# Kernel tuning notes

Measured on AMD Instinct MI355X. Metric: run time of the kernel, lower is better.

## Reference

```python
import jax, jax.numpy as jnp
import numpy as np

N, E, D, H, C, L = 100000, 1280000, 64, 4, 16, 3  # nodes, edges, dim, heads, head_dim, layers
NEG_SLOPE = 0.2
LN_EPS = 1e-5


def setup_inputs() -> dict:
    key = jax.random.key(0)
    ks = jax.random.split(key, 6)
    scale = 1.0 / np.sqrt(D)
    x = jax.random.normal(ks[0], (N, D), dtype=jnp.float32)
    edge_index = jax.random.randint(ks[1], (2, E), 0, N, dtype=jnp.int64)
    Wl = jax.random.normal(ks[2], (L, D, H * C), dtype=jnp.float32) * scale  # lin_l (source)
    Wr = jax.random.normal(ks[3], (L, D, H * C), dtype=jnp.float32) * scale  # lin_r (target)
    att = jax.random.normal(ks[4], (L, H, C), dtype=jnp.float32) * scale
    bias = jnp.zeros((L, H * C), dtype=jnp.float32)
    gamma = jnp.ones((L, D), dtype=jnp.float32)
    beta = jnp.zeros((L, D), dtype=jnp.float32)
    return dict(x=x, edge_index=edge_index, Wl=Wl, Wr=Wr, att=att, bias=bias, gamma=gamma, beta=beta)


def _gatv2_conv(x, src, dst, Wl, Wr, att, bias):
    # GATv2Conv (concat=True, share_weights=False, negative_slope=0.2)
    n = x.shape[0]
    xl = (x @ Wl).reshape(n, H, C)  # messages from source nodes
    xr = (x @ Wr).reshape(n, H, C)  # target-side transform
    m = xl[src] + xr[dst]  # [E', H, C]
    e = jnp.einsum('ehc,hc->eh', jax.nn.leaky_relu(m, NEG_SLOPE), att)  # [E', H]
    emax = jax.ops.segment_max(e, dst, num_segments=n)
    p = jnp.exp(e - emax[dst])
    denom = jax.ops.segment_sum(p, dst, num_segments=n)
    alpha = p / denom[dst]  # self-loops guarantee denom > 0
    out = jax.ops.segment_sum(alpha[:, :, None] * xl[src], dst, num_segments=n)  # [N, H, C]
    return out.reshape(n, H * C) + bias


def _layernorm(x, gamma, beta):
    mu = jnp.mean(x, axis=-1, keepdims=True)
    var = jnp.mean(jnp.square(x - mu), axis=-1, keepdims=True)
    return (x - mu) * jax.lax.rsqrt(var + LN_EPS) * gamma + beta


def reference(x, edge_index, Wl, Wr, att, bias, gamma, beta):
    n = x.shape[0]
    loops = jnp.arange(n, dtype=edge_index.dtype)
    src = jnp.concatenate([edge_index[0], loops])  # PyG add_self_loops=True
    dst = jnp.concatenate([edge_index[1], loops])
    for i in range(L):
        x_res = x
        x = _gatv2_conv(x, src, dst, Wl[i], Wr[i], att[i], bias[i])
        x = x + x_res  # residual
        x = _layernorm(x, gamma[i], beta[i])
        x = jax.nn.gelu(x, approximate=False)
    return x
```

## Files before the change

kernel.cpp:

```cpp
#include <hip/hip_runtime.h>
#include <math.h>


#define SCAN_CHUNK 1024

typedef __attribute__((ext_vector_type(8))) short short8;
typedef __attribute__((ext_vector_type(4))) float f32x4;

static inline int cdiv(int a, int b) { return (a + b - 1) / b; }

__device__ __forceinline__ unsigned short bf16_rtn(float v) {
    unsigned u = __float_as_uint(v);
    return (unsigned short)((u + 0x7fffu + ((u >> 16) & 1u)) >> 16);
}


__global__ void csr_init(const unsigned int* __restrict__ ei, int* __restrict__ flag,
                         int* __restrict__ deg, int N) {
    int i = blockIdx.x * blockDim.x + threadIdx.x;
    if (i < N) deg[i] = 1;
    if (blockIdx.x == 0 && threadIdx.x < 64) {
        int nz = (ei[2 * threadIdx.x + 1] != 0u) ? 1 : 0;
        unsigned long long b = __ballot(nz);
        if (threadIdx.x == 0) *flag = (b == 0ull) ? 1 : 0;
    }
}

__global__ void hist_kernel(const int* __restrict__ ei, int E, const int* __restrict__ flag,
                            int* __restrict__ deg, int* __restrict__ pos) {
    int e = blockIdx.x * blockDim.x + threadIdx.x;
    if (e >= E) return;
    int is64 = *flag;
    int d = is64 ? ei[2 * (E + e)] : ei[E + e];
    pos[e] = atomicAdd(&deg[d], 1);
}

__global__ void scan_blocks(const int* __restrict__ deg, int* __restrict__ rowptr,
                            int* __restrict__ partials, int N) {
    __shared__ int sdata[256];
    int t = threadIdx.x;
    int idx0 = blockIdx.x * SCAN_CHUNK + t * 4;
    int v[4]; int sum = 0;
    #pragma unroll
    for (int i = 0; i < 4; ++i) {
        int ii = idx0 + i;
        v[i] = (ii < N) ? deg[ii] : 0;
        sum += v[i];
    }
    sdata[t] = sum;
    __syncthreads();
    for (int off = 1; off < 256; off <<= 1) {
        int val = 0;
        if (t >= off) val = sdata[t - off];
        __syncthreads();
        if (t >= off) sdata[t] += val;
        __syncthreads();
    }
    int run = (t > 0) ? sdata[t - 1] : 0;
    #pragma unroll
    for (int i = 0; i < 4; ++i) {
        int ii = idx0 + i;
        if (ii < N) rowptr[ii] = run;
        run += v[i];
    }
    if (t == 255) partials[blockIdx.x] = sdata[255];
}

__global__ void scan_partials_k(int* __restrict__ partials, int NB) {
    __shared__ int sd[256];
    int t = threadIdx.x;
    sd[t] = (t < NB) ? partials[t] : 0;
    __syncthreads();
    for (int off = 1; off < 256; off <<= 1) {
        int val = 0;
        if (t >= off) val = sd[t - off];
        __syncthreads();
        if (t >= off) sd[t] += val;
        __syncthreads();
    }
    if (t < NB) partials[t] = (t > 0) ? sd[t - 1] : 0;
}

__global__ void add_offsets(int* __restrict__ rowptr, const int* __restrict__ partials,
                            int N, int Etot) {
    int i = blockIdx.x * blockDim.x + threadIdx.x;
    if (i < N) rowptr[i] += partials[i / SCAN_CHUNK];
    if (i == 0) rowptr[N] = Etot;
}

__global__ void fill_csr(const int* __restrict__ ei, int E, int N, const int* __restrict__ flag,
                         const int* __restrict__ rowptr, const int* __restrict__ pos,
                         int* __restrict__ col) {
    int i = blockIdx.x * blockDim.x + threadIdx.x;
    if (i >= E + N) return;
    if (i < E) {
        int is64 = *flag;
        int s = is64 ? ei[2 * i] : ei[i];
        int d = is64 ? ei[2 * (E + i)] : ei[E + i];
        col[rowptr[d] + pos[i]] = s;
    } else {
        int nn = i - E;
        col[rowptr[nn]] = nn;
    }
}

__global__ void wprep_kernel(const float* __restrict__ Wl, const float* __restrict__ Wr,
                             unsigned short* __restrict__ Bh, int Lnum) {
    int t = blockIdx.x * blockDim.x + threadIdx.x;
    int total = Lnum * 2 * 4 * 2 * 64 * 8;
    if (t >= total) return;
    int j    = t & 7;
    int lane = (t >> 3) & 63;
    int kc   = (t >> 9) & 1;
    int ct   = (t >> 10) & 3;
    int h    = (t >> 12) & 1;
    int l    = t >> 13;
    const float* W = (h ? Wr : Wl) + (size_t)l * 4096;
    int k = kc * 32 + (lane >> 4) * 8 + j;
    int c = ct * 16 + (lane & 15);
    Bh[t] = bf16_rtn(W[k * 64 + c]);
}

__global__ __launch_bounds__(256) void transform_mfma(
    const float* __restrict__ x, const unsigned short* __restrict__ Bh,
    unsigned short* __restrict__ XL, float* __restrict__ XR, int N) {
    int lane = threadIdx.x & 63;
    int wid = (blockIdx.x * blockDim.x + threadIdx.x) >> 6;
    int nw = (gridDim.x * blockDim.x) >> 6;
    int half = wid & 1;

    const short8* Bh8 = (const short8*)Bh;
    short8 bh[4][2];
    #pragma unroll
    for (int ct = 0; ct < 4; ++ct)
        #pragma unroll
        for (int kc = 0; kc < 2; ++kc)
            bh[ct][kc] = Bh8[((half * 4 + ct) * 2 + kc) * 64 + lane];

    int r16 = lane & 15, kq = lane >> 4;
    int ngroups = N >> 4;

    for (int gidx = wid >> 1; gidx < ngroups; gidx += (nw >> 1)) {
        int n0 = gidx << 4;
        const float4* row = (const float4*)(x + (size_t)(n0 + r16) * 64);
        float4 f0 = row[2 * kq], f1 = row[2 * kq + 1];
        float4 f2 = row[8 + 2 * kq], f3 = row[8 + 2 * kq + 1];
        float fa[8] = {f0.x, f0.y, f0.z, f0.w, f1.x, f1.y, f1.z, f1.w};
        float fb[8] = {f2.x, f2.y, f2.z, f2.w, f3.x, f3.y, f3.z, f3.w};
        short8 ah0, ah1, al0, al1;
        #pragma unroll
        for (int j = 0; j < 8; ++j) {
            unsigned short h0 = bf16_rtn(fa[j]);
            unsigned short h1 = bf16_rtn(fb[j]);
            ah0[j] = (short)h0;
            ah1[j] = (short)h1;
            al0[j] = (short)bf16_rtn(fa[j] - __uint_as_float((unsigned)h0 << 16));
            al1[j] = (short)bf16_rtn(fb[j] - __uint_as_float((unsigned)h1 << 16));
        }

        f32x4 acc[4] = {};
        #pragma unroll
        for (int ct = 0; ct < 4; ++ct) {
            acc[ct] = __builtin_amdgcn_mfma_f32_16x16x32_bf16(ah0, bh[ct][0], acc[ct], 0, 0, 0);
            acc[ct] = __builtin_amdgcn_mfma_f32_16x16x32_bf16(ah1, bh[ct][1], acc[ct], 0, 0, 0);
        }
        if (half) {
            #pragma unroll
            for (int ct = 0; ct < 4; ++ct) {
                acc[ct] = __builtin_amdgcn_mfma_f32_16x16x32_bf16(al0, bh[ct][0], acc[ct], 0, 0, 0);
                acc[ct] = __builtin_amdgcn_mfma_f32_16x16x32_bf16(al1, bh[ct][1], acc[ct], 0, 0, 0);
            }
        }
        if (half) {
            #pragma unroll
            for (int ct = 0; ct < 4; ++ct)
                #pragma unroll
                for (int r = 0; r < 4; ++r)
                    XR[(size_t)(n0 + kq * 4 + r) * 64 + ct * 16 + r16] = acc[ct][r];
        } else {
            #pragma unroll
            for (int ct = 0; ct < 4; ++ct)
                #pragma unroll
                for (int r = 0; r < 4; ++r)
                    XL[(size_t)(n0 + kq * 4 + r) * 64 + ct * 16 + r16] = bf16_rtn(acc[ct][r]);
        }
    }
}

__global__ __launch_bounds__(512) void gat_gather_kernel(
    const unsigned short* __restrict__ XL, const float* __restrict__ XR,
    const float* __restrict__ x_res,
    const int* __restrict__ rowptr, const int* __restrict__ col,
    const float* __restrict__ att, const float* __restrict__ bias,
    const float* __restrict__ gamma, const float* __restrict__ beta,
    float* __restrict__ x_out, int N) {
    int wid = (blockIdx.x * blockDim.x + threadIdx.x) >> 6;
    if (wid >= N) return;
    int lane = threadIdx.x & 63;
    int g = lane >> 4;
    int c = lane & 15;
    const int n = wid;

    float4 xr = ((const float4*)(XR + (size_t)n * 64))[c];
    float4 av = ((const float4*)att)[c];
    int start = rowptr[n], end = rowptr[n + 1];
    const ushort4* XL4 = (const ushort4*)XL;

    float m = -1e30f, s = 0.f;
    float o0 = 0.f, o1 = 0.f, o2 = 0.f, o3 = 0.f;

    for (int base = start; base < end; base += 64) {
        int rem = end - base;
        int chunk = rem < 64 ? rem : 64;
        int cidx = base + lane;
        int cl = col[cidx < end ? cidx : end - 1];
        int iters = (chunk + 7) >> 3;
        for (int t = 0; t < iters; ++t) {
            int ia = 8 * t + g;
            int ib = ia + 4;
            int sa = __shfl(cl, ia);
            int sb = __shfl(cl, ib);
            ushort4 ha = XL4[(size_t)sa * 16 + c];
            ushort4 hb = XL4[(size_t)sb * 16 + c];
            float va0 = __uint_as_float((unsigned)ha.x << 16);
            float va1 = __uint_as_float((unsigned)ha.y << 16);
            float va2 = __uint_as_float((unsigned)ha.z << 16);
            float va3 = __uint_as_float((unsigned)ha.w << 16);
            float vb0 = __uint_as_float((unsigned)hb.x << 16);
            float vb1 = __uint_as_float((unsigned)hb.y << 16);
            float vb2 = __uint_as_float((unsigned)hb.z << 16);
            float vb3 = __uint_as_float((unsigned)hb.w << 16);
            float ta0 = va0 + xr.x; ta0 = fmaxf(ta0, 0.2f * ta0);
            float ta1 = va1 + xr.y; ta1 = fmaxf(ta1, 0.2f * ta1);
            float ta2 = va2 + xr.z; ta2 = fmaxf(ta2, 0.2f * ta2);
            float ta3 = va3 + xr.w; ta3 = fmaxf(ta3, 0.2f * ta3);
            float tb0 = vb0 + xr.x; tb0 = fmaxf(tb0, 0.2f * tb0);
            float tb1 = vb1 + xr.y; tb1 = fmaxf(tb1, 0.2f * tb1);
            float tb2 = vb2 + xr.z; tb2 = fmaxf(tb2, 0.2f * tb2);
            float tb3 = vb3 + xr.w; tb3 = fmaxf(tb3, 0.2f * tb3);
            float wa = ta0 * av.x;
            wa = fmaf(ta1, av.y, wa);
            wa = fmaf(ta2, av.z, wa);
            wa = fmaf(ta3, av.w, wa);
            float wb = tb0 * av.x;
            wb = fmaf(tb1, av.y, wb);
            wb = fmaf(tb2, av.z, wb);
            wb = fmaf(tb3, av.w, wb);
            wa += __shfl_xor(wa, 1);
            wa += __shfl_xor(wa, 2);
            wb += __shfl_xor(wb, 1);
            wb += __shfl_xor(wb, 2);
            wa = (ia < chunk) ? wa : -1e30f;
            wb = (ib < chunk) ? wb : -1e30f;
            float mn = fmaxf(fmaxf(m, wa), wb);
            float pa = __expf(wa - mn);
            float pb = __expf(wb - mn);
            float sc = __expf(m - mn);
            s = fmaf(s, sc, pa + pb);
            o0 = fmaf(o0, sc, fmaf(pa, va0, pb * vb0));
            o1 = fmaf(o1, sc, fmaf(pa, va1, pb * vb1));
            o2 = fmaf(o2, sc, fmaf(pa, va2, pb * vb2));
            o3 = fmaf(o3, sc, fmaf(pa, va3, pb * vb3));
            m = mn;
        }
    }

    #pragma unroll
    for (int mask = 16; mask <= 32; mask <<= 1) {
        float m2 = __shfl_xor(m, mask);
        float s2 = __shfl_xor(s, mask);
        float q0 = __shfl_xor(o0, mask);
        float q1 = __shfl_xor(o1, mask);
        float q2 = __shfl_xor(o2, mask);
        float q3 = __shfl_xor(o3, mask);
        float mn = fmaxf(m, m2);
        float sa = __expf(m - mn), sb = __expf(m2 - mn);
        s = s * sa + s2 * sb;
        o0 = o0 * sa + q0 * sb;
        o1 = o1 * sa + q1 * sb;
        o2 = o2 * sa + q2 * sb;
        o3 = o3 * sa + q3 * sb;
        m = mn;
    }

    float inv = 1.f / s;
    float4 bi = ((const float4*)bias)[c];
    float4 rs = ((const float4*)(x_res + (size_t)n * 64))[c];
    float g0 = fmaf(o0, inv, bi.x + rs.x);
    float g1 = fmaf(o1, inv, bi.y + rs.y);
    float g2 = fmaf(o2, inv, bi.z + rs.z);
    float g3 = fmaf(o3, inv, bi.w + rs.w);

    float loc = g0 + g1 + g2 + g3;
    #pragma unroll
    for (int mask = 1; mask < 16; mask <<= 1) loc += __shfl_xor(loc, mask);
    float mu = loc * (1.f / 64.f);
    float d0 = g0 - mu, d1 = g1 - mu, d2 = g2 - mu, d3 = g3 - mu;
    float vs = d0 * d0 + d1 * d1 + d2 * d2 + d3 * d3;
    #pragma unroll
    for (int mask = 1; mask < 16; mask <<= 1) vs += __shfl_xor(vs, mask);
    float rstd = rsqrtf(vs * (1.f / 64.f) + 1e-5f);
    float4 ga = ((const float4*)gamma)[c];
    float4 be = ((const float4*)beta)[c];
    float y0 = fmaf(d0 * rstd, ga.x, be.x);
    float y1 = fmaf(d1 * rstd, ga.y, be.y);
    float y2 = fmaf(d2 * rstd, ga.z, be.z);
    float y3 = fmaf(d3 * rstd, ga.w, be.w);

    const float k = 0.70710678118654752f;
    float z0 = 0.5f * y0 * (1.f + erff(y0 * k));
    float z1 = 0.5f * y1 * (1.f + erff(y1 * k));
    float z2 = 0.5f * y2 * (1.f + erff(y2 * k));
    float z3 = 0.5f * y3 * (1.f + erff(y3 * k));

    if (g == 0) {
        ((float4*)(x_out + (size_t)n * 64))[c] = make_float4(z0, z1, z2, z3);
    }
}


extern "C" void kernel_launch(void* const* d_in, const int* in_sizes, int n_in,
                              void* d_out, int out_size, void* d_ws, size_t ws_size,
                              hipStream_t stream) {
    const float* x0    = (const float*)d_in[0];
    const int*   ei    = (const int*)d_in[1];
    const float* Wl    = (const float*)d_in[2];
    const float* Wr    = (const float*)d_in[3];
    const float* att   = (const float*)d_in[4];
    const float* bias  = (const float*)d_in[5];
    const float* gamma = (const float*)d_in[6];
    const float* beta  = (const float*)d_in[7];
    float* out = (float*)d_out;

    const int N = in_sizes[0] / 64;
    const int E = in_sizes[1] / 2;
    const int Lnum = in_sizes[2] / (64 * 64);
    const int Etot = E + N;

    char* ws = (char*)d_ws;
    size_t off = 0;
    auto alloc = [&](size_t bytes) {
        void* p = ws + off;
        off = (off + bytes + 255) & ~(size_t)255;
        return p;
    };
    unsigned short* XLb = (unsigned short*)alloc((size_t)N * 64 * 2);
    float* XR     = (float*)alloc((size_t)N * 64 * 4);
    float* XA     = (float*)alloc((size_t)N * 64 * 4);
    unsigned short* Bh = (unsigned short*)alloc((size_t)Lnum * 8192 * 2);
    int* rowptr   = (int*)alloc((size_t)(N + 1) * 4);
    int* deg      = (int*)alloc((size_t)N * 4);
    int* pos      = (int*)alloc((size_t)E * 4);
    int* partials = (int*)alloc(1024 * 4);
    int* flag     = (int*)alloc(256);
    int* col      = (int*)alloc((size_t)Etot * 4);

    wprep_kernel<<<cdiv(Lnum * 8192, 256), 256, 0, stream>>>(Wl, Wr, Bh, Lnum);
    csr_init<<<cdiv(N, 256), 256, 0, stream>>>((const unsigned int*)ei, flag, deg, N);
    hist_kernel<<<cdiv(E, 256), 256, 0, stream>>>(ei, E, flag, deg, pos);
    int NB = cdiv(N, SCAN_CHUNK);
    scan_blocks<<<NB, 256, 0, stream>>>(deg, rowptr, partials, N);
    scan_partials_k<<<1, 256, 0, stream>>>(partials, NB);
    add_offsets<<<cdiv(N + 1, 256), 256, 0, stream>>>(rowptr, partials, N, Etot);
    fill_csr<<<cdiv(Etot, 256), 256, 0, stream>>>(ei, E, N, flag, rowptr, pos, col);

    const float* xcur = x0;
    for (int l = 0; l < Lnum; ++l) {
        transform_mfma<<<2048, 256, 0, stream>>>(
            xcur, Bh + (size_t)l * 8192, XLb, XR, N);
        float* xnext = (l == Lnum - 1) ? out : XA;
        gat_gather_kernel<<<cdiv(N * 64, 512), 512, 0, stream>>>(
            XLb, XR, xcur, rowptr, col,
            att + (size_t)l * 64, bias + (size_t)l * 64,
            gamma + (size_t)l * 64, beta + (size_t)l * 64,
            xnext, N);
        xcur = xnext;
    }
}
```

Before: 415.1 us.

## Store XL in fp32, drop online-softmax max tracking, single wave per node group

The transform kernel now computes both XL and XR in one wave using split-bf16 (hi+lo) MFMA for both, and stores XL as fp32 instead of bf16. The gather kernel reads fp32 XL directly, loads col indices per edge instead of shuffling, and removes the running-max rescaling from the softmax, exponentiating raw scores. This removes the max/rescale exps and shuffles but doubles XL gather bytes, and skipping max subtraction risks overflow for large attention logits. The transform grid also shrinks.

Measured after the change: 423.7 us. 1.02x slower.

```diff
diff --git a/kernel.cpp b/kernel.cpp
--- a/kernel.cpp
+++ b/kernel.cpp
@@ -123,24 +123,23 @@
 
 __global__ __launch_bounds__(256) void transform_mfma(
     const float* __restrict__ x, const unsigned short* __restrict__ Bh,
-    unsigned short* __restrict__ XL, float* __restrict__ XR, int N) {
+    float* __restrict__ XL, float* __restrict__ XR, int N) {
     int lane = threadIdx.x & 63;
     int wid = (blockIdx.x * blockDim.x + threadIdx.x) >> 6;
     int nw = (gridDim.x * blockDim.x) >> 6;
-    int half = wid & 1;
 
     const short8* Bh8 = (const short8*)Bh;
-    short8 bh[4][2];
-    #pragma unroll
-    for (int ct = 0; ct < 4; ++ct)
+    short8 bh[8][2];
+    #pragma unroll
+    for (int ct = 0; ct < 8; ++ct)
         #pragma unroll
         for (int kc = 0; kc < 2; ++kc)
-            bh[ct][kc] = Bh8[((half * 4 + ct) * 2 + kc) * 64 + lane];
+            bh[ct][kc] = Bh8[(ct * 2 + kc) * 64 + lane];
 
     int r16 = lane & 15, kq = lane >> 4;
     int ngroups = N >> 4;
 
-    for (int gidx = wid >> 1; gidx < ngroups; gidx += (nw >> 1)) {
+    for (int gidx = wid; gidx < ngroups; gidx += nw) {
         int n0 = gidx << 4;
         const float4* row = (const float4*)(x + (size_t)(n0 + r16) * 64);
         float4 f0 = row[2 * kq], f1 = row[2 * kq + 1];
@@ -158,37 +157,29 @@
             al1[j] = (short)bf16_rtn(fb[j] - __uint_as_float((unsigned)h1 << 16));
         }
 
-        f32x4 acc[4] = {};
-        #pragma unroll
-        for (int ct = 0; ct < 4; ++ct) {
+        f32x4 acc[8] = {};
+        #pragma unroll
+        for (int ct = 0; ct < 8; ++ct) {
             acc[ct] = __builtin_amdgcn_mfma_f32_16x16x32_bf16(ah0, bh[ct][0], acc[ct], 0, 0, 0);
             acc[ct] = __builtin_amdgcn_mfma_f32_16x16x32_bf16(ah1, bh[ct][1], acc[ct], 0, 0, 0);
+            acc[ct] = __builtin_amdgcn_mfma_f32_16x16x32_bf16(al0, bh[ct][0], acc[ct], 0, 0, 0);
+            acc[ct] = __builtin_amdgcn_mfma_f32_16x16x32_bf16(al1, bh[ct][1], acc[ct], 0, 0, 0);
         }
-        if (half) {
+        #pragma unroll
+        for (int ct = 0; ct < 4; ++ct)
             #pragma unroll
-            for (int ct = 0; ct < 4; ++ct) {
-                acc[ct] = __builtin_amdgcn_mfma_f32_16x16x32_bf16(al0, bh[ct][0], acc[ct], 0, 0, 0);
-                acc[ct] = __builtin_amdgcn_mfma_f32_16x16x32_bf16(al1, bh[ct][1], acc[ct], 0, 0, 0);
-            }
-        }
-        if (half) {
+            for (int r = 0; r < 4; ++r)
+                XL[(size_t)(n0 + kq * 4 + r) * 64 + ct * 16 + r16] = acc[ct][r];
+        #pragma unroll
+        for (int ct = 4; ct < 8; ++ct)
             #pragma unroll
-            for (int ct = 0; ct < 4; ++ct)
-                #pragma unroll
-                for (int r = 0; r < 4; ++r)
-                    XR[(size_t)(n0 + kq * 4 + r) * 64 + ct * 16 + r16] = acc[ct][r];
-        } else {
-            #pragma unroll
-            for (int ct = 0; ct < 4; ++ct)
-                #pragma unroll
-                for (int r = 0; r < 4; ++r)
-                    XL[(size_t)(n0 + kq * 4 + r) * 64 + ct * 16 + r16] = bf16_rtn(acc[ct][r]);
-        }
+            for (int r = 0; r < 4; ++r)
+                XR[(size_t)(n0 + kq * 4 + r) * 64 + (ct - 4) * 16 + r16] = acc[ct][r];
     }
 }
 
 __global__ __launch_bounds__(512) void gat_gather_kernel(
-    const unsigned short* __restrict__ XL, const float* __restrict__ XR,
+    const float* __restrict__ XL, const float* __restrict__ XR,
     const float* __restrict__ x_res,
     const int* __restrict__ rowptr, const int* __restrict__ col,
     const float* __restrict__ att, const float* __restrict__ bias,
@@ -204,83 +195,56 @@
     float4 xr = ((const float4*)(XR + (size_t)n * 64))[c];
     float4 av = ((const float4*)att)[c];
     int start = rowptr[n], end = rowptr[n + 1];
-    const ushort4* XL4 = (const ushort4*)XL;
-
-    float m = -1e30f, s = 0.f;
+    const float4* XL4 = (const float4*)XL;
+
+    float s = 0.f;
     float o0 = 0.f, o1 = 0.f, o2 = 0.f, o3 = 0.f;
 
-    for (int base = start; base < end; base += 64) {
-        int rem = end - base;
-        int chunk = rem < 64 ? rem : 64;
-        int cidx = base + lane;
-        int cl = col[cidx < end ? cidx : end - 1];
-        int iters = (chunk + 7) >> 3;
-        for (int t = 0; t < iters; ++t) {
-            int ia = 8 * t + g;
-            int ib = ia + 4;
-            int sa = __shfl(cl, ia);
-            int sb = __shfl(cl, ib);
-            ushort4 ha = XL4[(size_t)sa * 16 + c];
-            ushort4 hb = XL4[(size_t)sb * 16 + c];
-            float va0 = __uint_as_float((unsigned)ha.x << 16);
-            float va1 = __uint_as_float((unsigned)ha.y << 16);
-            float va2 = __uint_as_float((unsigned)ha.z << 16);
-            float va3 = __uint_as_float((unsigned)ha.w << 16);
-            float vb0 = __uint_as_float((unsigned)hb.x << 16);
-            float vb1 = __uint_as_float((unsigned)hb.y << 16);
-            float vb2 = __uint_as_float((unsigned)hb.z << 16);
-            float vb3 = __uint_as_float((unsigned)hb.w << 16);
-            float ta0 = va0 + xr.x; ta0 = fmaxf(ta0, 0.2f * ta0);
-            float ta1 = va1 + xr.y; ta1 = fmaxf(ta1, 0.2f * ta1);
-            float ta2 = va2 + xr.z; ta2 = fmaxf(ta2, 0.2f * ta2);
-            float ta3 = va3 + xr.w; ta3 = fmaxf(ta3, 0.2f * ta3);
-            float tb0 = vb0 + xr.x; tb0 = fmaxf(tb0, 0.2f * tb0);
-            float tb1 = vb1 + xr.y; tb1 = fmaxf(tb1, 0.2f * tb1);
-            float tb2 = vb2 + xr.z; tb2 = fmaxf(tb2, 0.2f * tb2);
-            float tb3 = vb3 + xr.w; tb3 = fmaxf(tb3, 0.2f * tb3);
-            float wa = ta0 * av.x;
-            wa = fmaf(ta1, av.y, wa);
-            wa = fmaf(ta2, av.z, wa);
-            wa = fmaf(ta3, av.w, wa);
-            float wb = tb0 * av.x;
-            wb = fmaf(tb1, av.y, wb);
-            wb = fmaf(tb2, av.z, wb);
-            wb = fmaf(tb3, av.w, wb);
-            wa += __shfl_xor(wa, 1);
-            wa += __shfl_xor(wa, 2);
-            wb += __shfl_xor(wb, 1);
-            wb += __shfl_xor(wb, 2);
-            wa = (ia < chunk) ? wa : -1e30f;
-            wb = (ib < chunk) ? wb : -1e30f;
-            float mn = fmaxf(fmaxf(m, wa), wb);
-            float pa = __expf(wa - mn);
-            float pb = __expf(wb - mn);
-            float sc = __expf(m - mn);
-            s = fmaf(s, sc, pa + pb);
-            o0 = fmaf(o0, sc, fmaf(pa, va0, pb * vb0));
-            o1 = fmaf(o1, sc, fmaf(pa, va1, pb * vb1));
-            o2 = fmaf(o2, sc, fmaf(pa, va2, pb * vb2));
-            o3 = fmaf(o3, sc, fmaf(pa, va3, pb * vb3));
-            m = mn;
-        }
+    for (int k0 = start; k0 < end; k0 += 8) {
+        int ka = k0 + g;
+        int kb = ka + 4;
+        int sa = col[ka < end ? ka : end - 1];
+        int sb = col[kb < end ? kb : end - 1];
+        float4 va = XL4[(size_t)sa * 16 + c];
+        float4 vb = XL4[(size_t)sb * 16 + c];
+        float ta0 = va.x + xr.x; ta0 = fmaxf(ta0, 0.2f * ta0);
+        float ta1 = va.y + xr.y; ta1 = fmaxf(ta1, 0.2f * ta1);
+        float ta2 = va.z + xr.z; ta2 = fmaxf(ta2, 0.2f * ta2);
+        float ta3 = va.w + xr.w; ta3 = fmaxf(ta3, 0.2f * ta3);
+        float tb0 = vb.x + xr.x; tb0 = fmaxf(tb0, 0.2f * tb0);
+        float tb1 = vb.y + xr.y; tb1 = fmaxf(tb1, 0.2f * tb1);
+        float tb2 = vb.z + xr.z; tb2 = fmaxf(tb2, 0.2f * tb2);
+        float tb3 = vb.w + xr.w; tb3 = fmaxf(tb3, 0.2f * tb3);
+        float wa = ta0 * av.x;
+        wa = fmaf(ta1, av.y, wa);
+        wa = fmaf(ta2, av.z, wa);
+        wa = fmaf(ta3, av.w, wa);
+        float wb = tb0 * av.x;
+        wb = fmaf(tb1, av.y, wb);
+        wb = fmaf(tb2, av.z, wb);
+        wb = fmaf(tb3, av.w, wb);
+        wa += __shfl_xor(wa, 1);
+        wa += __shfl_xor(wa, 2);
+        wb += __shfl_xor(wb, 1);
+        wb += __shfl_xor(wb, 2);
+        wa = (ka < end) ? wa : -1e30f;
+        wb = (kb < end) ? wb : -1e30f;
+        float pa = __expf(wa);
+        float pb = __expf(wb);
+        s += pa + pb;
+        o0 = fmaf(pa, va.x, o0); o0 = fmaf(pb, vb.x, o0);
+        o1 = fmaf(pa, va.y, o1); o1 = fmaf(pb, vb.y, o1);
+        o2 = fmaf(pa, va.z, o2); o2 = fmaf(pb, vb.z, o2);
+        o3 = fmaf(pa, va.w, o3); o3 = fmaf(pb, vb.w, o3);
     }
 
     #pragma unroll
     for (int mask = 16; mask <= 32; mask <<= 1) {
-        float m2 = __shfl_xor(m, mask);
-        float s2 = __shfl_xor(s, mask);
-        float q0 = __shfl_xor(o0, mask);
-        float q1 = __shfl_xor(o1, mask);
-        float q2 = __shfl_xor(o2, mask);
-        float q3 = __shfl_xor(o3, mask);
-        float mn = fmaxf(m, m2);
-        float sa = __expf(m - mn), sb = __expf(m2 - mn);
-        s = s * sa + s2 * sb;
-        o0 = o0 * sa + q0 * sb;
-        o1 = o1 * sa + q1 * sb;
-        o2 = o2 * sa + q2 * sb;
-        o3 = o3 * sa + q3 * sb;
-        m = mn;
+        s  += __shfl_xor(s, mask);
+        o0 += __shfl_xor(o0, mask);
+        o1 += __shfl_xor(o1, mask);
+        o2 += __shfl_xor(o2, mask);
+        o3 += __shfl_xor(o3, mask);
     }
 
     float inv = 1.f / s;
@@ -344,7 +308,7 @@
         off = (off + bytes + 255) & ~(size_t)255;
         return p;
     };
-    unsigned short* XLb = (unsigned short*)alloc((size_t)N * 64 * 2);
+    float* XLf    = (float*)alloc((size_t)N * 64 * 4);
     float* XR     = (float*)alloc((size_t)N * 64 * 4);
     float* XA     = (float*)alloc((size_t)N * 64 * 4);
     unsigned short* Bh = (unsigned short*)alloc((size_t)Lnum * 8192 * 2);
@@ -366,11 +330,11 @@
 
     const float* xcur = x0;
     for (int l = 0; l < Lnum; ++l) {
-        transform_mfma<<<2048, 256, 0, stream>>>(
-            xcur, Bh + (size_t)l * 8192, XLb, XR, N);
+        transform_mfma<<<1600, 256, 0, stream>>>(
+            xcur, Bh + (size_t)l * 8192, XLf, XR, N);
         float* xnext = (l == Lnum - 1) ? out : XA;
         gat_gather_kernel<<<cdiv(N * 64, 512), 512, 0, stream>>>(
-            XLb, XR, xcur, rowptr, col,
+            XLf, XR, xcur, rowptr, col,
             att + (size_t)l * 64, bias + (size_t)l * 64,
             gamma + (size_t)l * 64, beta + (size_t)l * 64,
             xnext, N);
```
